# Kernel tuning notes

Hardware: AMD Instinct MI355X
Metric: run time of the kernel (lower is better)

## Reference

```python
import jax, jax.numpy as jnp
import numpy as np

E = 256        # embed_size
H = 512        # nHidden (== coverage d)
EN_V = 32000   # en_vocab
HI_V = 32000   # hi_vocab
S = 96         # source length
T = 96         # target length


def setup_inputs() -> dict:
    key = jax.random.key(0)
    ks = jax.random.split(key, 26)
    def p(k, shape, scale=0.05):
        return jax.random.normal(k, shape, dtype=jnp.float32) * scale
    return dict(
        in_seq=jax.random.randint(ks[0], (S,), 0, EN_V),
        out_seq=jax.random.randint(ks[1], (T,), 0, HI_V),
        enc_embed=p(ks[2], (EN_V, E)),
        dec_embed=p(ks[3], (HI_V, E)),
        # encoder bidirectional GRU (forward / backward directions)
        Wih_f=p(ks[4], (3 * H, E)), Whh_f=p(ks[5], (3 * H, H)), bih_f=p(ks[6], (3 * H,)), bhh_f=p(ks[7], (3 * H,)),
        Wih_b=p(ks[8], (3 * H, E)), Whh_b=p(ks[9], (3 * H, H)), bih_b=p(ks[10], (3 * H,)), bhh_b=p(ks[11], (3 * H,)),
        # decoder GRU (input E + 2H)
        Wih_d=p(ks[12], (3 * H, E + 2 * H)), Whh_d=p(ks[13], (3 * H, H)), bih_d=p(ks[14], (3 * H,)), bhh_d=p(ks[15], (3 * H,)),
        # coverage tanh-RNN (input 3H -> H)
        Wih_c=p(ks[16], (H, 3 * H)), Whh_c=p(ks[17], (H, H)), bih_c=p(ks[18], (H,)), bhh_c=p(ks[19], (H,)),
        # attention params
        va=p(ks[20], (H,)), wa=p(ks[21], (H, H)), ua=p(ks[22], (H, 2 * H)), vc=p(ks[23], (H, H)),
        # output projection (2H + H -> hi_vocab)
        lin_W=p(ks[24], (HI_V, 3 * H)), lin_b=p(ks[25], (HI_V,)),
    )


def _gru_cell(x, h, Wih, Whh, bih, bhh):
    # torch GRU gate order: r, z, n
    gi = Wih @ x + bih
    gh = Whh @ h + bhh
    ir, iz, in_ = jnp.split(gi, 3)
    hr, hz, hn = jnp.split(gh, 3)
    r = jax.nn.sigmoid(ir + hr)
    z = jax.nn.sigmoid(iz + hz)
    n = jnp.tanh(in_ + r * hn)
    return (1.0 - z) * n + z * h


def _forward(in_seq, out_seq, enc_embed, dec_embed,
             Wih_f, Whh_f, bih_f, bhh_f, Wih_b, Whh_b, bih_b, bhh_b,
             Wih_d, Whh_d, bih_d, bhh_d, Wih_c, Whh_c, bih_c, bhh_c,
             va, wa, ua, vc, lin_W, lin_b):
    x_enc = enc_embed[in_seq]                      # (S, E)
    h0 = jnp.zeros((H,), x_enc.dtype)

    def f_step(h, x):
        h2 = _gru_cell(x, h, Wih_f, Whh_f, bih_f, bhh_f)
        return h2, h2

    def b_step(h, x):
        h2 = _gru_cell(x, h, Wih_b, Whh_b, bih_b, bhh_b)
        return h2, h2

    h_fwd, out_f = jax.lax.scan(f_step, h0, x_enc)
    _, out_b = jax.lax.scan(b_step, h0, x_enc[::-1])
    enc = jnp.concatenate([out_f, out_b[::-1]], axis=-1)   # (S, 2H)
    ua_enc = enc @ ua.T                                     # (S, H), reused every step

    def attention(dec_h, cov_vec):
        pre = wa @ dec_h + ua_enc                           # (S, H)
        if cov_vec is not None:
            pre = pre + cov_vec @ vc.T
        e = jnp.tanh(pre) @ va                              # (S,)
        alpha = jax.nn.softmax(e)
        ctx = alpha @ enc                                   # (2H,)
        return ctx, alpha

    def coverage(dec_h, alpha, cov_last):
        # per-position input: alpha_s * [enc_s ; dec_h]  -> (S, 3H)
        inp = alpha[:, None] * jnp.concatenate(
            [enc, jnp.broadcast_to(dec_h, (S, H))], axis=-1)

        def c_step(h, x):
            h2 = jnp.tanh(Wih_c @ x + bih_c + Whh_c @ h + bhh_c)
            return h2, h2

        h_last, outs = jax.lax.scan(c_step, jnp.zeros((H,), inp.dtype), inp)
        # drop last output, prepend previous last_coverage, tanh (as in source)
        cov_vec = jnp.tanh(jnp.concatenate([cov_last[None, :], outs[:-1]], axis=0))
        return cov_vec, h_last

    dec_emb = dec_embed[out_seq]                            # (T, E)

    # --- initial decode step (uses encoder final forward hidden) ---
    h_enc = h_fwd
    ctx0, alpha0 = attention(h_enc, None)
    x0 = jnp.concatenate([ctx0, dec_emb[0]])
    h1 = _gru_cell(x0, h_enc, Wih_d, Whh_d, bih_d, bhh_d)
    out0 = lin_W @ jnp.concatenate([h1, ctx0]) + lin_b
    # note: source discards h1 for the loop; coverage also uses the encoder hidden
    cov_vec0, cov_last0 = coverage(h_enc, alpha0, jnp.zeros((H,), enc.dtype))

    def dec_step(carry, emb):
        h, cov_last, cov_vec = carry
        ctx, alpha = attention(h, cov_vec)
        x = jnp.concatenate([ctx, emb])
        h2 = _gru_cell(x, h, Wih_d, Whh_d, bih_d, bhh_d)
        logits = lin_W @ jnp.concatenate([h2, ctx]) + lin_b
        cov_vec2, cov_last2 = coverage(h2, alpha, cov_last)
        return (h2, cov_last2, cov_vec2), logits

    _, outs = jax.lax.scan(dec_step, (h_enc, cov_last0, cov_vec0), dec_emb[1:])
    return jnp.concatenate([out0[None, :], outs], axis=0)   # (T, HI_V)


def reference(in_seq, out_seq, enc_embed, dec_embed,
              Wih_f, Whh_f, bih_f, bhh_f, Wih_b, Whh_b, bih_b, bhh_b,
              Wih_d, Whh_d, bih_d, bhh_d, Wih_c, Whh_c, bih_c, bhh_c,
              va, wa, ua, vc, lin_W, lin_b):
    return _forward(in_seq, out_seq, enc_embed, dec_embed,
                    Wih_f, Whh_f, bih_f, bhh_f, Wih_b, Whh_b, bih_b, bhh_b,
                    Wih_d, Whh_d, bih_d, bhh_d, Wih_c, Whh_c, bih_c, bhh_c,
                    va, wa, ua, vc, lin_W, lin_b)
```

## Files before the change

kernel.cpp:

```cpp
#include <hip/hip_runtime.h>
#include <hip/hip_bf16.h>
#include <hip/hip_fp16.h>
#include <math.h>

#define CS 96
#define CT 96
#define CE 256
#define CH 512
#define CH2 1024
#define CH3 1536
#define CV 32000
#define CXD 1280

typedef unsigned int u32;
typedef unsigned short u16;
typedef unsigned long long u64;
typedef __attribute__((ext_vector_type(4))) int i32x4;

__device__ __forceinline__ float sigm(float x){ return 1.f/(1.f+expf(-x)); }

__device__ __forceinline__ float dot2f(u32 a, u32 b, float c){
#if __has_builtin(__builtin_amdgcn_fdot2)
  typedef _Float16 hv2 __attribute__((ext_vector_type(2)));
  hv2 x = __builtin_bit_cast(hv2, a), y = __builtin_bit_cast(hv2, b);
  return __builtin_amdgcn_fdot2(x, y, c, false);
#else
  __half2 x = __builtin_bit_cast(__half2, a), y = __builtin_bit_cast(__half2, b);
  return c + __half2float(x.x)*__half2float(y.x) + __half2float(x.y)*__half2float(y.y);
#endif
}

__device__ __forceinline__ u32 packh2(float a, float b){
  return (u32)__half_as_ushort(__float2half(a)) | ((u32)__half_as_ushort(__float2half(b)) << 16);
}

__device__ __forceinline__ float spinf(const u64* p, u32 want){
  u64 x; int g = 0;
  do { x = __hip_atomic_load(p, __ATOMIC_RELAXED, __HIP_MEMORY_SCOPE_AGENT); }
  while ((u32)(x>>32) < want && ++g < 200000);
  return __uint_as_float((u32)x);
}
__device__ __forceinline__ void tagstore(u64* p, u32 tag, float v){
  __hip_atomic_store(p, ((u64)tag<<32) | (u64)__float_as_uint(v),
                     __ATOMIC_RELAXED, __HIP_MEMORY_SCOPE_AGENT);
}

#define COVBAR() do{ asm volatile("s_waitcnt lgkmcnt(0)" ::: "memory"); \
                     __builtin_amdgcn_sched_barrier(0); \
                     __builtin_amdgcn_s_barrier(); \
                     __builtin_amdgcn_sched_barrier(0); }while(0)

__global__ void k_init(u64* tags, int ntags, float* cov_last){
  int i = blockIdx.x*blockDim.x + threadIdx.x;
  int stride = gridDim.x*blockDim.x;
  for (int j=i; j<ntags; j+=stride) tags[j] = 0ull;
  for (int j=i; j<CH; j+=stride) cov_last[j] = 0.f;
}

__global__ void k_embed(const int* iseq, const int* oseq, const float* ee, const float* de,
                        float* x_enc, float* x_dec){
  int s = blockIdx.x, d = threadIdx.x;
  x_enc[s*CE+d] = ee[(long)iseq[s]*CE + d];
  x_dec[s*CE+d] = de[(long)oseq[s]*CE + d];
}

__global__ void k_gi(const float* Wf, const float* bf, const float* Wb, const float* bb,
                     const float* x_enc, float* gf, float* gb){
  int idx = blockIdx.x*256 + threadIdx.x;
  int dir = idx / (CS*CH3);
  int rem = idx - dir*(CS*CH3);
  int s = rem / CH3, r = rem - s*CH3;
  const float* W = dir ? Wb : Wf;
  const float* b = dir ? bb : bf;
  const float* x = x_enc + s*CE;
  const float* w = W + (long)r*CE;
  float acc = b[r];
  #pragma unroll 8
  for (int k=0;k<CE;k++) acc += w[k]*x[k];
  (dir ? gb : gf)[s*CH3 + r] = acc;
}

__launch_bounds__(512)
__global__ void k_enc_f(const float* Whf, const float* bhf, const float* Whb, const float* bhb,
                        const float* gf, const float* gb, float* outf, float* outb, u64* hx){
  int b = blockIdx.x, tid = threadIdx.x;
  int dir = b >> 3;
  const float* Whh = dir ? Whb : Whf;
  const float* bhh = dir ? bhb : bhf;
  const float* gi  = dir ? gb : gf;
  float* o = dir ? outb : outf;
  u64* hxd = hx + (size_t)dir*CH;
  int jl = (b&7)*64 + (tid>>3);
  int part = tid&7, c0 = part*64;
  __shared__ float hl[CH];

  for (int s=0;s<CS;s++){
    if (s > 0){
      if (tid < 64){
        #pragma unroll
        for (int i=0;i<8;i++){ int idx = i*64+tid; hl[idx] = spinf(&hxd[idx], (u32)s); }
      }
      __syncthreads();
    }
    int pos = dir ? (CS-1-s) : s;
    float ar=0.f, az=0.f, an=0.f;
    if (s > 0){
      const float* wr = Whh + (size_t)jl*CH;
      const float* wz = Whh + (size_t)(jl+CH)*CH;
      const float* wn = Whh + (size_t)(jl+2*CH)*CH;
      #pragma unroll 4
      for (int k=c0;k<c0+64;k++){
        float h = hl[k];
        ar += wr[k]*h; az += wz[k]*h; an += wn[k]*h;
      }
    }
    ar += __shfl_xor(ar,1); ar += __shfl_xor(ar,2); ar += __shfl_xor(ar,4);
    az += __shfl_xor(az,1); az += __shfl_xor(az,2); az += __shfl_xor(az,4);
    an += __shfl_xor(an,1); an += __shfl_xor(an,2); an += __shfl_xor(an,4);
    if (part == 0){
      const float* g = gi + pos*CH3;
      float hpj = (s>0) ? hl[jl] : 0.f;
      float r = sigm(g[jl]       + ar + bhh[jl]);
      float z = sigm(g[jl+CH]    + az + bhh[jl+CH]);
      float n = tanhf(g[jl+2*CH] + r*(an + bhh[jl+2*CH]));
      float h = (1.f-z)*n + z*hpj;
      o[pos*CH + jl] = h;
      tagstore(&hxd[jl], (u32)(s+1), h);
    }
    __syncthreads();
  }
}

__global__ void k_prep2(const float* ua, const float* Wic, const float* outf, const float* outb,
                        float* ua_enc, float* Aenc, float* h_carry){
  int idx = blockIdx.x*256 + threadIdx.x;
  if (idx < 2*CS*CH){
    int which = idx / (CS*CH);
    int rem = idx - which*(CS*CH);
    int s = rem / CH, r = rem - s*CH;
    const float* of = outf + s*CH;
    const float* ob = outb + s*CH;
    const float* w = which ? (Wic + (long)r*CH3) : (ua + (long)r*CH2);
    float acc = 0.f;
    #pragma unroll 4
    for (int k=0;k<CH;k++) acc += w[k]*of[k];
    #pragma unroll 4
    for (int k=0;k<CH;k++) acc += w[CH+k]*ob[k];
    (which ? Aenc : ua_enc)[s*CH + r] = acc;
  } else if (idx < 2*CS*CH + CH){
    int j = idx - 2*CS*CH;
    h_carry[j] = outf[(CS-1)*CH + j];
  }
}

__global__ void k_cvt(const float* w, u16* o, int n){
  int i = blockIdx.x*blockDim.x + threadIdx.x;
  int stride = gridDim.x*blockDim.x;
  for (; i<n; i+=stride){
    union { float f; u32 u; } v; v.f = w[i];
    u32 r = (v.u + 0x7fffu + ((v.u>>16)&1u)) >> 16;
    o[i] = (u16)r;
  }
}

__global__ void k_cvt_cov(const float* Wic, u32* wic16P){
  int i = blockIdx.x*256 + threadIdx.x;
  int kp = i >> 9, r = i & 511;
  float a = Wic[(size_t)r*CH3 + CH2 + 2*kp];
  float b = Wic[(size_t)r*CH3 + CH2 + 2*kp + 1];
  wic16P[(size_t)kp*512 + r] = packh2(a, b);
}

__global__ void k_quant(const float* Whc, uint4* w8m, float* rs){
  int r = blockIdx.x;
  int l = threadIdx.x;
  const float* wr = Whc + (size_t)r*CH;
  float m = 0.f;
  for (int k=l; k<CH; k+=64) m = fmaxf(m, fabsf(wr[k]));
  for (int d=1; d<64; d<<=1) m = fmaxf(m, __shfl_xor(m,d));
  float sc = (m > 0.f) ? (127.f/m) : 0.f;
  if (l < 32){
    int kb = l>>2, q = l&3;
    u32 wv[4];
    #pragma unroll
    for (int wi=0;wi<4;wi++){
      u32 p = 0;
      #pragma unroll
      for (int j=0;j<4;j++){
        int v = (int)rintf(wr[kb*64 + q*16 + wi*4 + j]*sc);
        v = max(-127, min(127, v));
        p |= (u32)(v & 255) << (8*j);
      }
      wv[wi] = p;
    }
    int tile = (r>>4)*8 + kb;
    int lane = q*16 + (r&15);
    w8m[(size_t)tile*64 + lane] = make_uint4(wv[0],wv[1],wv[2],wv[3]);
  }
  if (l==0) rs[r] = m/(127.f*127.f);
}

__global__ void k_wah(const float* wa, const float* h, float* wah){
  int j = blockIdx.x*64 + (threadIdx.x>>2);
  int c0 = (threadIdx.x&3)*128;
  const float* w = wa + (long)j*CH;
  float acc = 0.f;
  #pragma unroll 4
  for (int k=c0;k<c0+128;k++) acc += w[k]*h[k];
  acc += __shfl_xor(acc,1); acc += __shfl_xor(acc,2);
  if ((threadIdx.x&3)==0) wah[j] = acc;
}

__global__ void k_attn0(const float* va, const float* ua_enc, const float* wah, float* e){
  int s = blockIdx.x, tid = threadIdx.x;
  __shared__ float red[4];
  float sum = 0.f;
  #pragma unroll
  for (int jj=0;jj<2;jj++){
    int j = tid + jj*256;
    float acc = ua_enc[s*CH + j] + wah[j];
    sum += va[j]*tanhf(acc);
  }
  for (int m=1;m<64;m<<=1) sum += __shfl_xor(sum,m);
  if ((tid&63)==0) red[tid>>6] = sum;
  __syncthreads();
  if (tid==0) e[s] = red[0]+red[1]+red[2]+red[3];
}

template<int BF16>
__launch_bounds__(512, 2)
__global__ void k_step(int t, const void* Wv, const float* lb, const float* hE,
                       u64* hc64, const float* x_dec,
                       const float* eR, float* eW,
                       const float* outf, const float* outb,
                       const float* wa, const float* vc, const float* va, const float* ua_enc,
                       const float* Wid, const float* bid, const float* Whd, const float* bhd,
                       const uint4* w8m, const float* rs, const u32* wic16P,
                       const float* bic, const float* bhc, const float* Aenc,
                       u64* cv64, float* cov_last, float* out){
  int b = blockIdx.x, tid = threadIdx.x;
  u32 wantH = (u32)(t+1);
  u64* hcW = hc64 + (size_t)(t&1)*CH;
  const u64* hcR = hc64 + (size_t)((t+1)&1)*CH;

  __shared__ float el[CS], al[CS];
  __shared__ float ctxl[CH2];
  __shared__ float hl[CH];
  __shared__ float he2[CH];
  __shared__ float red[8];
  __shared__ u32 part_l[CH];
  __shared__ __align__(16) u32 h8w[128];
  __shared__ u32 hd16[256];
  __shared__ float cvsl[CH];

  if (tid < CS) el[tid] = eR[tid];
  __syncthreads();
  if (tid == 0){
    float m = -1e30f;
    for (int s=0;s<CS;s++) m = fmaxf(m, el[s]);
    float sm = 0.f;
    for (int s=0;s<CS;s++){ float ex = expf(el[s]-m); al[s] = ex; sm += ex; }
    float inv = 1.f/sm;
    for (int s=0;s<CS;s++) al[s] *= inv;
  }
  __syncthreads();
  if (b != 0){
    float a0=0.f, a1=0.f;
    for (int s=0;s<CS;s++){ a0 += al[s]*outf[s*CH+tid]; a1 += al[s]*outb[s*CH+tid]; }
    ctxl[tid] = a0; ctxl[CH+tid] = a1;
  }

  if (b == 0){
    if (t == 0){ if (tid < CH) hl[tid] = hE[tid]; }
    else if (tid < 64){
      #pragma unroll
      for (int i=0;i<8;i++){ int idx=i*64+tid; hl[idx] = spinf(&hcW[idx], wantH); }
    }
    __syncthreads();
    if (tid < 256) hd16[tid] = packh2(hl[2*tid], hl[2*tid+1]);
    __syncthreads();
    float bacc_r = 0.f;
    {
      const u32* bw = wic16P + tid;
      #pragma unroll 8
      for (int kp=0;kp<256;kp++)
        bacc_r = dot2f(bw[(size_t)kp*512], hd16[kp], bacc_r);
    }
    i32x4 af[4][8];
    {
      int w = tid>>6, l = tid&63;
      const i32x4* wp = (const i32x4*)w8m;
      #pragma unroll
      for (int j=0;j<4;j++){
        #pragma unroll
        for (int kb=0;kb<8;kb++)
          af[j][kb] = wp[((size_t)((4*w+j)*8+kb))*64 + l];
        asm volatile("" ::: "memory");
      }
    }
    float bsum_r = bic[tid] + bhc[tid];
    float rs_r = rs[tid];
    float a_next = Aenc[tid];
    tagstore(&cv64[tid], wantH, tanhf(cov_last[tid]));
    __syncthreads();

    int w = tid>>6, l = tid&63;
    for (int s=0;s<CS;s++){
      if (s > 0){
        i32x4 acc0={0,0,0,0}, acc1={0,0,0,0}, acc2={0,0,0,0}, acc3={0,0,0,0};
        #pragma unroll
        for (int kb=0;kb<8;kb++){
          i32x4 bfr = *(const i32x4*)&h8w[kb*16 + (l>>4)*4];
          acc0 = __builtin_amdgcn_mfma_i32_16x16x64_i8(af[0][kb], bfr, acc0, 0,0,0);
          acc1 = __builtin_amdgcn_mfma_i32_16x16x64_i8(af[1][kb], bfr, acc1, 0,0,0);
          acc2 = __builtin_amdgcn_mfma_i32_16x16x64_i8(af[2][kb], bfr, acc2, 0,0,0);
          acc3 = __builtin_amdgcn_mfma_i32_16x16x64_i8(af[3][kb], bfr, acc3, 0,0,0);
        }
        if ((l & 15) == 0){
          int rq = l >> 4;
          *(i32x4*)&part_l[(4*w+0)*16 + rq*4] = acc0;
          *(i32x4*)&part_l[(4*w+1)*16 + rq*4] = acc1;
          *(i32x4*)&part_l[(4*w+2)*16 + rq*4] = acc2;
          *(i32x4*)&part_l[(4*w+3)*16 + rq*4] = acc3;
        }
      }
      COVBAR();
      {
        float T = (s > 0) ? (float)(int)part_l[tid] * rs_r : 0.f;
        float a_cur = a_next;
        if (s < CS-1) a_next = Aenc[(s+1)*CH + tid];
        float h = tanhf(T + al[s]*(a_cur + bacc_r) + bsum_r);
        if (s < CS-1){
          int q = (int)rintf(h * 127.f);
          u32 bq = (u32)(q & 255);
          u32 p01 = bq | (__shfl_xor(bq,1) << 8);
          u32 p = p01 | (__shfl_xor(p01,2) << 16);
          if ((tid & 3) == 0) h8w[tid >> 2] = p;
          tagstore(&cv64[(size_t)(s+1)*CH + tid], wantH, tanhf(h));
        } else {
          cov_last[tid] = h;
        }
      }
      COVBAR();
    }
    return;
  }

  if (b >= 97){
    if (t <= 1){ if (tid < CH) he2[tid] = hE[tid]; }
    else       { if (tid < CH) he2[tid] = __uint_as_float((u32)hcR[tid]); }
    __syncthreads();
    {
      int j = (b-97)*16 + (tid>>5);
      int ln = tid&31;
      const float* xd = x_dec + t*CE;
      float ar=0.f, az=0.f, an=0.f;
      {
        int c0 = ln*40;
        const float* wr = Wid + (size_t)j*CXD;
        const float* wz = Wid + (size_t)(j+CH)*CXD;
        const float* wn = Wid + (size_t)(j+2*CH)*CXD;
        for (int k=c0;k<c0+40;k++){
          float x = (k<CH2) ? ctxl[k] : xd[k-CH2];
          ar += wr[k]*x; az += wz[k]*x; an += wn[k]*x;
        }
      }
      float hr=0.f, hz=0.f, hn2=0.f;
      {
        int c0 = ln*16;
        const float* wr = Whd + (size_t)j*CH;
        const float* wz = Whd + (size_t)(j+CH)*CH;
        const float* wn = Whd + (size_t)(j+2*CH)*CH;
        for (int k=c0;k<c0+16;k++){
          float hv = he2[k];
          hr += wr[k]*hv; hz += wz[k]*hv; hn2 += wn[k]*hv;
        }
      }
      for (int m=1;m<32;m<<=1){
        ar+=__shfl_xor(ar,m); az+=__shfl_xor(az,m); an+=__shfl_xor(an,m);
        hr+=__shfl_xor(hr,m); hz+=__shfl_xor(hz,m); hn2+=__shfl_xor(hn2,m);
      }
      if (ln==0){
        float hprev = he2[j];
        float r = sigm(ar + bid[j]       + hr + bhd[j]);
        float z = sigm(az + bid[j+CH]    + hz + bhd[j+CH]);
        float n = tanhf(an + bid[j+2*CH] + r*(hn2 + bhd[j+2*CH]));
        tagstore(&hcW[j], wantH, (1.f-z)*n + z*hprev);
      }
    }
    if (tid < 64){
      #pragma unroll
      for (int i=0;i<8;i++){ int idx=i*64+tid; hl[idx] = spinf(&hcW[idx], wantH); }
    }
    __syncthreads();
    {
      int ln = tid&63;
      int gw = (b-97)*8 + (tid>>6);
      float x[24];
      #pragma unroll
      for (int k=0;k<24;k++){
        int c = k*64 + ln;
        x[k] = (c<CH) ? hl[c] : ctxl[c];
      }
      #pragma unroll
      for (int k=0;k<24;k++){
        int c = k*64 + ln;
        x[k] = (c<CH) ? hl[c] : ctxl[c-CH];
      }
      for (int r=24000+gw; r<CV; r+=256){
        float acc = 0.f;
        if (BF16){
          const u16* w = (const u16*)Wv + (size_t)r*CH3;
          #pragma unroll
          for (int k=0;k<24;k++){
            u32 u = (u32)w[k*64+ln] << 16;
            acc += __uint_as_float(u)*x[k];
          }
        } else {
          const float* w = (const float*)Wv + (size_t)r*CH3;
          #pragma unroll
          for (int k=0;k<24;k++) acc += w[k*64+ln]*x[k];
        }
        for (int m=1;m<64;m<<=1) acc += __shfl_xor(acc,m);
        if (ln==0) out[(size_t)t*CV + r] = acc + lb[r];
      }
    }
    return;
  }

  int s = b - 1;
  if (t == 0){ if (tid < CH) he2[tid] = hE[tid]; }
  if (tid < 64){
    #pragma unroll
    for (int i=0;i<8;i++){ int idx=i*64+tid; hl[idx] = spinf(&hcW[idx], wantH); }
  }
  __syncthreads();
  {
    int ln = tid&63;
    int gw = (b-1)*8 + (tid>>6);
    float x[24];
    #pragma unroll
    for (int k=0;k<24;k++){
      int c = k*64 + ln;
      x[k] = (c<CH) ? hl[c] : ctxl[c-CH];
    }
    for (int r=gw; r<24000; r+=768){
      float acc = 0.f;
      if (BF16){
        const u16* w = (const u16*)Wv + (size_t)r*CH3;
        #pragma unroll
        for (int k=0;k<24;k++){
          u32 u = (u32)w[k*64+ln] << 16;
          acc += __uint_as_float(u)*x[k];
        }
      } else {
        const float* w = (const float*)Wv + (size_t)r*CH3;
        #pragma unroll
        for (int k=0;k<24;k++) acc += w[k*64+ln]*x[k];
      }
      for (int m=1;m<64;m<<=1) acc += __shfl_xor(acc,m);
      if (ln==0) out[(size_t)t*CV + r] = acc + lb[r];
    }
  }
  if (tid < 64){
    #pragma unroll
    for (int i=0;i<8;i++){ int idx=i*64+tid; cvsl[idx] = spinf(&cv64[(size_t)s*CH+idx], wantH); }
  }
  __syncthreads();
  {
    int j = tid;
    const float* hw = (t==0) ? he2 : hl;
    const float* wr = wa + (size_t)j*CH;
    float wacc = 0.f;
    #pragma unroll 4
    for (int k=0;k<CH;k++) wacc += wr[k]*hw[k];
    float acc = ua_enc[s*CH + j] + wacc;
    const float* v = vc + (size_t)j*CH;
    #pragma unroll 4
    for (int k=0;k<CH;k++) acc += v[k]*cvsl[k];
    float val = va[j]*tanhf(acc);
    for (int m=1;m<64;m<<=1) val += __shfl_xor(val,m);
    if ((tid&63)==0) red[tid>>6] = val;
    __syncthreads();
    if (tid==0){
      float sm = 0.f;
      #pragma unroll
      for (int i=0;i<8;i++) sm += red[i];
      eW[s] = sm;
    }
  }
}

extern "C" void kernel_launch(void* const* d_in, const int* in_sizes, int n_in,
                              void* d_out, int out_size, void* d_ws, size_t ws_size,
                              hipStream_t stream){
  (void)in_sizes; (void)n_in; (void)out_size;
  const int*   iseq = (const int*)d_in[0];
  const int*   oseq = (const int*)d_in[1];
  const float* ee   = (const float*)d_in[2];
  const float* de   = (const float*)d_in[3];
  const float* Wih_f=(const float*)d_in[4];  const float* Whh_f=(const float*)d_in[5];
  const float* bih_f=(const float*)d_in[6];  const float* bhh_f=(const float*)d_in[7];
  const float* Wih_b=(const float*)d_in[8];  const float* Whh_b=(const float*)d_in[9];
  const float* bih_b=(const float*)d_in[10]; const float* bhh_b=(const float*)d_in[11];
  const float* Wih_d=(const float*)d_in[12]; const float* Whh_d=(const float*)d_in[13];
  const float* bih_d=(const float*)d_in[14]; const float* bhh_d=(const float*)d_in[15];
  const float* Wih_c=(const float*)d_in[16]; const float* Whh_c=(const float*)d_in[17];
  const float* bih_c=(const float*)d_in[18]; const float* bhh_c=(const float*)d_in[19];
  const float* va   =(const float*)d_in[20]; const float* wa   =(const float*)d_in[21];
  const float* ua   =(const float*)d_in[22]; const float* vc   =(const float*)d_in[23];
  const float* lin_W=(const float*)d_in[24]; const float* lin_b=(const float*)d_in[25];
  float* out = (float*)d_out;
  char* ws = (char*)d_ws;

  size_t off = 0;
  auto A = [&](size_t bytes){ size_t r = off; off = (off + bytes + 255) & ~(size_t)255; return r; };
  size_t o_w8m   = A((size_t)CH*128*4);
  size_t o_rs    = A((size_t)CH*4);
  size_t o_wicP  = A((size_t)256*512*4);
  size_t o_tags  = A((size_t)(1024 + 1024 + CS*CH)*8);
  size_t o_xenc = A((size_t)CS*CE*4), o_xdec = A((size_t)CT*CE*4);
  size_t o_gf   = A((size_t)CS*CH3*4), o_gb  = A((size_t)CS*CH3*4);
  size_t o_of   = A((size_t)CS*CH*4),  o_ob  = A((size_t)CS*CH*4);
  size_t o_uae  = A((size_t)CS*CH*4),  o_Ae  = A((size_t)CS*CH*4);
  size_t o_e0   = A(CS*4), o_e1 = A(CS*4);
  size_t o_hE   = A(CH*4), o_cl = A(CH*4);
  size_t o_wah  = A(CH*4);
  size_t o_lwb  = A((size_t)CV*CH3*2);
  bool use16 = (off <= ws_size);

  uint4* w8m = (uint4*)(ws+o_w8m);    float* rs = (float*)(ws+o_rs);
  u32* wic16P = (u32*)(ws+o_wicP);
  u64* tags = (u64*)(ws+o_tags);
  u64* hx   = tags;
  u64* hc64 = tags + 1024;
  u64* cv64 = tags + 2048;
  int ntags = 1024 + 1024 + CS*CH;
  float* x_enc = (float*)(ws+o_xenc); float* x_dec = (float*)(ws+o_xdec);
  float* gf = (float*)(ws+o_gf);      float* gb = (float*)(ws+o_gb);
  float* outf = (float*)(ws+o_of);    float* outb = (float*)(ws+o_ob);
  float* ua_enc = (float*)(ws+o_uae); float* Aenc = (float*)(ws+o_Ae);
  float* eb0 = (float*)(ws+o_e0);     float* eb1 = (float*)(ws+o_e1);
  float* hE = (float*)(ws+o_hE);      float* cov_last = (float*)(ws+o_cl);
  float* wah = (float*)(ws+o_wah);
  u16* lwb = (u16*)(ws+o_lwb);

  k_init<<<64,256,0,stream>>>(tags, ntags, cov_last);
  k_embed<<<CS,256,0,stream>>>(iseq, oseq, ee, de, x_enc, x_dec);
  k_gi<<<(2*CS*CH3)/256,256,0,stream>>>(Wih_f,bih_f,Wih_b,bih_b,x_enc,gf,gb);
  k_cvt_cov<<<(256*512)/256,256,0,stream>>>(Wih_c, wic16P);
  k_quant<<<CH,64,0,stream>>>(Whh_c, w8m, rs);
  if (use16)
    k_cvt<<<2048,256,0,stream>>>(lin_W, lwb, CV*CH3);
  k_enc_f<<<16,512,0,stream>>>(Whh_f,bhh_f,Whh_b,bhh_b, gf,gb, outf,outb, hx);
  k_prep2<<<(2*CS*CH+CH)/256,256,0,stream>>>(ua, Wih_c, outf, outb, ua_enc, Aenc, hE);
  k_wah<<<8,256,0,stream>>>(wa, hE, wah);
  k_attn0<<<CS,256,0,stream>>>(va, ua_enc, wah, eb0);

  const void* Wv = use16 ? (const void*)lwb : (const void*)lin_W;
  for (int t=0;t<CT;t++){
    const float* eR = (t&1) ? eb1 : eb0;
    float*       eW = (t&1) ? eb0 : eb1;
    if (use16)
      k_step<1><<<129,512,0,stream>>>(t, Wv, lin_b, hE, hc64, x_dec, eR, eW,
                                      outf, outb, wa, vc, va, ua_enc,
                                      Wih_d, bih_d, Whh_d, bhh_d,
                                      w8m, rs, wic16P, bih_c, bhh_c, Aenc,
                                      cv64, cov_last, out);
    else
      k_step<0><<<129,512,0,stream>>>(t, Wv, lin_b, hE, hc64, x_dec, eR, eW,
                                      outf, outb, wa, vc, va, ua_enc,
                                      Wih_d, bih_d, Whh_d, bhh_d,
                                      w8m, rs, wic16P, bih_c, bhh_c, Aenc,
                                      cv64, cov_last, out);
  }
}
```

Before: 23.88 ms.

## Fuse per-timestep decoder launches into one persistent kernel with tagged flags

Replaces 96 separate k_step launches with a single persistent k_dec kernel of 256 blocks that loops over timesteps. Cross-step dependencies go through tagged atomic flags (attention energies now stored as tagged u64 values, hidden state read by spinning). The int8 coverage weight fragments are loaded into registers once instead of every step, and the output-projection rows are split across more blocks. The encoder recurrence also switches to float4 loads with a padded shared hidden buffer. This removes per-step launch and kernel-boundary overhead, but relies on all 256 blocks being co-resident and on spin-wait correctness; the spin limit is also halved.

```diff
diff --git a/kernel.cpp b/kernel.cpp
--- a/kernel.cpp
+++ b/kernel.cpp
@@ -37,7 +37,7 @@
 __device__ __forceinline__ float spinf(const u64* p, u32 want){
   u64 x; int g = 0;
   do { x = __hip_atomic_load(p, __ATOMIC_RELAXED, __HIP_MEMORY_SCOPE_AGENT); }
-  while ((u32)(x>>32) < want && ++g < 200000);
+  while ((u32)(x>>32) < want && ++g < 100000);
   return __uint_as_float((u32)x);
 }
 __device__ __forceinline__ void tagstore(u64* p, u32 tag, float v){
@@ -92,26 +92,30 @@
   u64* hxd = hx + (size_t)dir*CH;
   int jl = (b&7)*64 + (tid>>3);
   int part = tid&7, c0 = part*64;
-  __shared__ float hl[CH];
+  __shared__ __align__(16) float hl[544];
 
   for (int s=0;s<CS;s++){
     if (s > 0){
       if (tid < 64){
         #pragma unroll
-        for (int i=0;i<8;i++){ int idx = i*64+tid; hl[idx] = spinf(&hxd[idx], (u32)s); }
+        for (int i=0;i<8;i++) hl[i*68+tid] = spinf(&hxd[i*64+tid], (u32)s);
       }
       __syncthreads();
     }
     int pos = dir ? (CS-1-s) : s;
     float ar=0.f, az=0.f, an=0.f;
     if (s > 0){
-      const float* wr = Whh + (size_t)jl*CH;
-      const float* wz = Whh + (size_t)(jl+CH)*CH;
-      const float* wn = Whh + (size_t)(jl+2*CH)*CH;
-      #pragma unroll 4
-      for (int k=c0;k<c0+64;k++){
-        float h = hl[k];
-        ar += wr[k]*h; az += wz[k]*h; an += wn[k]*h;
+      const float4* wr = (const float4*)(Whh + (size_t)jl*CH + c0);
+      const float4* wz = (const float4*)(Whh + (size_t)(jl+CH)*CH + c0);
+      const float4* wn = (const float4*)(Whh + (size_t)(jl+2*CH)*CH + c0);
+      const float4* hp = (const float4*)&hl[part*68];
+      #pragma unroll
+      for (int k=0;k<16;k++){
+        float4 h = hp[k];
+        float4 a = wr[k], z = wz[k], n = wn[k];
+        ar += a.x*h.x + a.y*h.y + a.z*h.z + a.w*h.w;
+        az += z.x*h.x + z.y*h.y + z.z*h.z + z.w*h.w;
+        an += n.x*h.x + n.y*h.y + n.z*h.z + n.w*h.w;
       }
     }
     ar += __shfl_xor(ar,1); ar += __shfl_xor(ar,2); ar += __shfl_xor(ar,4);
@@ -119,7 +123,7 @@
     an += __shfl_xor(an,1); an += __shfl_xor(an,2); an += __shfl_xor(an,4);
     if (part == 0){
       const float* g = gi + pos*CH3;
-      float hpj = (s>0) ? hl[jl] : 0.f;
+      float hpj = (s>0) ? hl[jl + ((jl>>6)<<2)] : 0.f;
       float r = sigm(g[jl]       + ar + bhh[jl]);
       float z = sigm(g[jl+CH]    + az + bhh[jl+CH]);
       float n = tanhf(g[jl+2*CH] + r*(an + bhh[jl+2*CH]));
@@ -211,7 +215,7 @@
   if ((threadIdx.x&3)==0) wah[j] = acc;
 }
 
-__global__ void k_attn0(const float* va, const float* ua_enc, const float* wah, float* e){
+__global__ void k_attn0(const float* va, const float* ua_enc, const float* wah, u64* e64){
   int s = blockIdx.x, tid = threadIdx.x;
   __shared__ float red[4];
   float sum = 0.f;
@@ -224,24 +228,20 @@
   for (int m=1;m<64;m<<=1) sum += __shfl_xor(sum,m);
   if ((tid&63)==0) red[tid>>6] = sum;
   __syncthreads();
-  if (tid==0) e[s] = red[0]+red[1]+red[2]+red[3];
+  if (tid==0) tagstore(&e64[s], 1u, red[0]+red[1]+red[2]+red[3]);
 }
 
 template<int BF16>
 __launch_bounds__(512, 2)
-__global__ void k_step(int t, const void* Wv, const float* lb, const float* hE,
-                       u64* hc64, const float* x_dec,
-                       const float* eR, float* eW,
-                       const float* outf, const float* outb,
-                       const float* wa, const float* vc, const float* va, const float* ua_enc,
-                       const float* Wid, const float* bid, const float* Whd, const float* bhd,
-                       const uint4* w8m, const float* rs, const u32* wic16P,
-                       const float* bic, const float* bhc, const float* Aenc,
-                       u64* cv64, float* cov_last, float* out){
+__global__ void k_dec(const void* Wv, const float* lb, const float* hE,
+                      u64* hc64, const float* x_dec, u64* e64,
+                      const float* outf, const float* outb,
+                      const float* wa, const float* vc, const float* va, const float* ua_enc,
+                      const float* Wid, const float* bid, const float* Whd, const float* bhd,
+                      const uint4* w8m, const float* rs, const u32* wic16P,
+                      const float* bic, const float* bhc, const float* Aenc,
+                      u64* cv64, float* cov_last, float* out){
   int b = blockIdx.x, tid = threadIdx.x;
-  u32 wantH = (u32)(t+1);
-  u64* hcW = hc64 + (size_t)(t&1)*CH;
-  const u64* hcR = hc64 + (size_t)((t+1)&1)*CH;
 
   __shared__ float el[CS], al[CS];
   __shared__ float ctxl[CH2];
@@ -253,240 +253,297 @@
   __shared__ u32 hd16[256];
   __shared__ float cvsl[CH];
 
-  if (tid < CS) el[tid] = eR[tid];
-  __syncthreads();
-  if (tid == 0){
-    float m = -1e30f;
-    for (int s=0;s<CS;s++) m = fmaxf(m, el[s]);
-    float sm = 0.f;
-    for (int s=0;s<CS;s++){ float ex = expf(el[s]-m); al[s] = ex; sm += ex; }
-    float inv = 1.f/sm;
-    for (int s=0;s<CS;s++) al[s] *= inv;
+  if (tid < CH) he2[tid] = hE[tid];
+
+  i32x4 af[4][8];
+  if (b == 0){
+    int w = tid>>6, l = tid&63;
+    const i32x4* wp = (const i32x4*)w8m;
+    #pragma unroll
+    for (int j=0;j<4;j++){
+      #pragma unroll
+      for (int kb=0;kb<8;kb++)
+        af[j][kb] = wp[((size_t)((4*w+j)*8+kb))*64 + l];
+      asm volatile("" ::: "memory");
+    }
   }
   __syncthreads();
-  if (b != 0){
-    float a0=0.f, a1=0.f;
-    for (int s=0;s<CS;s++){ a0 += al[s]*outf[s*CH+tid]; a1 += al[s]*outb[s*CH+tid]; }
-    ctxl[tid] = a0; ctxl[CH+tid] = a1;
-  }
-
-  if (b == 0){
-    if (t == 0){ if (tid < CH) hl[tid] = hE[tid]; }
-    else if (tid < 64){
-      #pragma unroll
-      for (int i=0;i<8;i++){ int idx=i*64+tid; hl[idx] = spinf(&hcW[idx], wantH); }
-    }
+
+  for (int t=0;t<CT;t++){
+    u32 wantH = (u32)(t+1);
+    u64* hcW = hc64 + (size_t)(t&1)*CH;
+    const u64* hcR = hc64 + (size_t)((t+1)&1)*CH;
+    const u64* eR = e64 + (size_t)(t&1)*CS;
+    u64* eW = e64 + (size_t)((t+1)&1)*CS;
+
+    if (tid < CS) el[tid] = spinf(&eR[tid], wantH);
     __syncthreads();
-    if (tid < 256) hd16[tid] = packh2(hl[2*tid], hl[2*tid+1]);
+    if (tid == 0){
+      float m = -1e30f;
+      for (int s=0;s<CS;s++) m = fmaxf(m, el[s]);
+      float sm = 0.f;
+      for (int s=0;s<CS;s++){ float ex = expf(el[s]-m); al[s] = ex; sm += ex; }
+      float inv = 1.f/sm;
+      for (int s=0;s<CS;s++) al[s] *= inv;
+    }
     __syncthreads();
-    float bacc_r = 0.f;
+
+    if (b == 0){
+      if (t == CT-1) break;
+      if (t == 0){ if (tid < CH) hl[tid] = he2[tid]; }
+      else if (tid < 64){
+        #pragma unroll
+        for (int i=0;i<8;i++){ int idx=i*64+tid; hl[idx] = spinf(&hcW[idx], wantH); }
+      }
+      __syncthreads();
+      if (tid < 256) hd16[tid] = packh2(hl[2*tid], hl[2*tid+1]);
+      __syncthreads();
+      float bacc_r = 0.f;
+      {
+        const u32* bw = wic16P + tid;
+        #pragma unroll 8
+        for (int kp=0;kp<256;kp++)
+          bacc_r = dot2f(bw[(size_t)kp*512], hd16[kp], bacc_r);
+      }
+      float bsum_r = bic[tid] + bhc[tid];
+      float rs_r = rs[tid];
+      float a_next = Aenc[tid];
+      tagstore(&cv64[tid], wantH, tanhf(cov_last[tid]));
+      __syncthreads();
+
+      int w = tid>>6, l = tid&63;
+      for (int s=0;s<CS;s++){
+        if (s > 0){
+          i32x4 acc0={0,0,0,0}, acc1={0,0,0,0}, acc2={0,0,0,0}, acc3={0,0,0,0};
+          #pragma unroll
+          for (int kb=0;kb<8;kb++){
+            i32x4 bfr = *(const i32x4*)&h8w[kb*16 + (l>>4)*4];
+            acc0 = __builtin_amdgcn_mfma_i32_16x16x64_i8(af[0][kb], bfr, acc0, 0,0,0);
+            acc1 = __builtin_amdgcn_mfma_i32_16x16x64_i8(af[1][kb], bfr, acc1, 0,0,0);
+            acc2 = __builtin_amdgcn_mfma_i32_16x16x64_i8(af[2][kb], bfr, acc2, 0,0,0);
+            acc3 = __builtin_amdgcn_mfma_i32_16x16x64_i8(af[3][kb], bfr, acc3, 0,0,0);
+          }
+          if ((l & 15) == 0){
+            int rq = l >> 4;
+            *(i32x4*)&part_l[(4*w+0)*16 + rq*4] = acc0;
+            *(i32x4*)&part_l[(4*w+1)*16 + rq*4] = acc1;
+            *(i32x4*)&part_l[(4*w+2)*16 + rq*4] = acc2;
+            *(i32x4*)&part_l[(4*w+3)*16 + rq*4] = acc3;
+          }
+        }
+        COVBAR();
+        {
+          float T = (s > 0) ? (float)(int)part_l[tid] * rs_r : 0.f;
+          float a_cur = a_next;
+          if (s < CS-1) a_next = Aenc[(s+1)*CH + tid];
+          float h = tanhf(T + al[s]*(a_cur + bacc_r) + bsum_r);
+          if (s < CS-1){
+            int q = (int)rintf(h * 127.f);
+            u32 bq = (u32)(q & 255);
+            u32 p01 = bq | (__shfl_xor(bq,1) << 8);
+            u32 p = p01 | (__shfl_xor(p01,2) << 16);
+            if ((tid & 3) == 0) h8w[tid >> 2] = p;
+            tagstore(&cv64[(size_t)(s+1)*CH + tid], wantH, tanhf(h));
+          } else {
+            cov_last[tid] = h;
+          }
+        }
+        COVBAR();
+      }
+      __syncthreads();
+      continue;
+    }
+
     {
-      const u32* bw = wic16P + tid;
-      #pragma unroll 8
-      for (int kp=0;kp<256;kp++)
-        bacc_r = dot2f(bw[(size_t)kp*512], hd16[kp], bacc_r);
-    }
-    i32x4 af[4][8];
+      float a0=0.f, a1=0.f;
+      for (int s=0;s<CS;s++){ a0 += al[s]*outf[s*CH+tid]; a1 += al[s]*outb[s*CH+tid]; }
+      ctxl[tid] = a0; ctxl[CH+tid] = a1;
+    }
+    __syncthreads();
+
+    if (b >= 97 && b <= 128){
+      if (t >= 2){
+        if (tid < 64){
+          #pragma unroll
+          for (int i=0;i<8;i++){ int idx=i*64+tid; he2[idx] = spinf(&hcR[idx], (u32)t); }
+        }
+        __syncthreads();
+      }
+      {
+        int j = (b-97)*16 + (tid>>5);
+        int ln = tid&31;
+        const float* xd = x_dec + t*CE;
+        float ar=0.f, az=0.f, an=0.f;
+        {
+          int c0 = ln*40;
+          const float* wr = Wid + (size_t)j*CXD;
+          const float* wz = Wid + (size_t)(j+CH)*CXD;
+          const float* wn = Wid + (size_t)(j+2*CH)*CXD;
+          for (int k=c0;k<c0+40;k++){
+            float x = (k<CH2) ? ctxl[k] : xd[k-CH2];
+            ar += wr[k]*x; az += wz[k]*x; an += wn[k]*x;
+          }
+        }
+        float hr=0.f, hz=0.f, hn2=0.f;
+        {
+          int c0 = ln*16;
+          const float* wr = Whd + (size_t)j*CH;
+          const float* wz = Whd + (size_t)(j+CH)*CH;
+          const float* wn = Whd + (size_t)(j+2*CH)*CH;
+          for (int k=c0;k<c0+16;k++){
+            float hv = he2[k];
+            hr += wr[k]*hv; hz += wz[k]*hv; hn2 += wn[k]*hv;
+          }
+        }
+        for (int m=1;m<32;m<<=1){
+          ar+=__shfl_xor(ar,m); az+=__shfl_xor(az,m); an+=__shfl_xor(an,m);
+          hr+=__shfl_xor(hr,m); hz+=__shfl_xor(hz,m); hn2+=__shfl_xor(hn2,m);
+        }
+        if (ln==0){
+          float hprev = he2[j];
+          float r = sigm(ar + bid[j]       + hr + bhd[j]);
+          float z = sigm(az + bid[j+CH]    + hz + bhd[j+CH]);
+          float n = tanhf(an + bid[j+2*CH] + r*(hn2 + bhd[j+2*CH]));
+          tagstore(&hcW[j], wantH, (1.f-z)*n + z*hprev);
+        }
+      }
+      if (tid < 64){
+        #pragma unroll
+        for (int i=0;i<8;i++){ int idx=i*64+tid; hl[idx] = spinf(&hcW[idx], wantH); }
+      }
+      __syncthreads();
+      {
+        int ln = tid&63;
+        int gw = (b-97)*8 + (tid>>6);
+        float x[24];
+        #pragma unroll
+        for (int k=0;k<24;k++){
+          int c = k*64 + ln;
+          x[k] = (c<CH) ? hl[c] : ctxl[c-CH];
+        }
+        for (int r=12288+gw; r<16384; r+=256){
+          float acc = 0.f;
+          if (BF16){
+            const u16* w = (const u16*)Wv + (size_t)r*CH3;
+            #pragma unroll
+            for (int k=0;k<24;k++){
+              u32 u = (u32)w[k*64+ln] << 16;
+              acc += __uint_as_float(u)*x[k];
+            }
+          } else {
+            const float* w = (const float*)Wv + (size_t)r*CH3;
+            #pragma unroll
+            for (int k=0;k<24;k++) acc += w[k*64+ln]*x[k];
+          }
+          for (int m=1;m<64;m<<=1) acc += __shfl_xor(acc,m);
+          if (ln==0) out[(size_t)t*CV + r] = acc + lb[r];
+        }
+      }
+      __syncthreads();
+      continue;
+    }
+
+    if (b >= 129){
+      if (tid < 64){
+        #pragma unroll
+        for (int i=0;i<8;i++){ int idx=i*64+tid; hl[idx] = spinf(&hcW[idx], wantH); }
+      }
+      __syncthreads();
+      {
+        int ln = tid&63;
+        int gw = (b-129)*8 + (tid>>6);
+        float x[24];
+        #pragma unroll
+        for (int k=0;k<24;k++){
+          int c = k*64 + ln;
+          x[k] = (c<CH) ? hl[c] : ctxl[c-CH];
+        }
+        for (int r=16384+gw; r<CV; r+=1016){
+          float acc = 0.f;
+          if (BF16){
+            const u16* w = (const u16*)Wv + (size_t)r*CH3;
+            #pragma unroll
+            for (int k=0;k<24;k++){
+              u32 u = (u32)w[k*64+ln] << 16;
+              acc += __uint_as_float(u)*x[k];
+            }
+          } else {
+            const float* w = (const float*)Wv + (size_t)r*CH3;
+            #pragma unroll
+            for (int k=0;k<24;k++) acc += w[k*64+ln]*x[k];
+          }
+          for (int m=1;m<64;m<<=1) acc += __shfl_xor(acc,m);
+          if (ln==0) out[(size_t)t*CV + r] = acc + lb[r];
+        }
+      }
+      __syncthreads();
+      continue;
+    }
+
     {
-      int w = tid>>6, l = tid&63;
-      const i32x4* wp = (const i32x4*)w8m;
-      #pragma unroll
-      for (int j=0;j<4;j++){
-        #pragma unroll
-        for (int kb=0;kb<8;kb++)
-          af[j][kb] = wp[((size_t)((4*w+j)*8+kb))*64 + l];
-        asm volatile("" ::: "memory");
-      }
-    }
-    float bsum_r = bic[tid] + bhc[tid];
-    float rs_r = rs[tid];
-    float a_next = Aenc[tid];
-    tagstore(&cv64[tid], wantH, tanhf(cov_last[tid]));
-    __syncthreads();
-
-    int w = tid>>6, l = tid&63;
-    for (int s=0;s<CS;s++){
-      if (s > 0){
-        i32x4 acc0={0,0,0,0}, acc1={0,0,0,0}, acc2={0,0,0,0}, acc3={0,0,0,0};
-        #pragma unroll
-        for (int kb=0;kb<8;kb++){
-          i32x4 bfr = *(const i32x4*)&h8w[kb*16 + (l>>4)*4];
-          acc0 = __builtin_amdgcn_mfma_i32_16x16x64_i8(af[0][kb], bfr, acc0, 0,0,0);
-          acc1 = __builtin_amdgcn_mfma_i32_16x16x64_i8(af[1][kb], bfr, acc1, 0,0,0);
-          acc2 = __builtin_amdgcn_mfma_i32_16x16x64_i8(af[2][kb], bfr, acc2, 0,0,0);
-          acc3 = __builtin_amdgcn_mfma_i32_16x16x64_i8(af[3][kb], bfr, acc3, 0,0,0);
-        }
-        if ((l & 15) == 0){
-          int rq = l >> 4;
-          *(i32x4*)&part_l[(4*w+0)*16 + rq*4] = acc0;
-          *(i32x4*)&part_l[(4*w+1)*16 + rq*4] = acc1;
-          *(i32x4*)&part_l[(4*w+2)*16 + rq*4] = acc2;
-          *(i32x4*)&part_l[(4*w+3)*16 + rq*4] = acc3;
-        }
-      }
-      COVBAR();
+      int s = b - 1;
+      if (tid < 64){
+        #pragma unroll
+        for (int i=0;i<8;i++){ int idx=i*64+tid; hl[idx] = spinf(&hcW[idx], wantH); }
+      }
+      __syncthreads();
       {
-        float T = (s > 0) ? (float)(int)part_l[tid] * rs_r : 0.f;
-        float a_cur = a_next;
-        if (s < CS-1) a_next = Aenc[(s+1)*CH + tid];
-        float h = tanhf(T + al[s]*(a_cur + bacc_r) + bsum_r);
-        if (s < CS-1){
-          int q = (int)rintf(h * 127.f);
-          u32 bq = (u32)(q & 255);
-          u32 p01 = bq | (__shfl_xor(bq,1) << 8);
-          u32 p = p01 | (__shfl_xor(p01,2) << 16);
-          if ((tid & 3) == 0) h8w[tid >> 2] = p;
-          tagstore(&cv64[(size_t)(s+1)*CH + tid], wantH, tanhf(h));
-        } else {
-          cov_last[tid] = h;
-        }
-      }
-      COVBAR();
-    }
-    return;
-  }
-
-  if (b >= 97){
-    if (t <= 1){ if (tid < CH) he2[tid] = hE[tid]; }
-    else       { if (tid < CH) he2[tid] = __uint_as_float((u32)hcR[tid]); }
-    __syncthreads();
-    {
-      int j = (b-97)*16 + (tid>>5);
-      int ln = tid&31;
-      const float* xd = x_dec + t*CE;
-      float ar=0.f, az=0.f, an=0.f;
-      {
-        int c0 = ln*40;
-        const float* wr = Wid + (size_t)j*CXD;
-        const float* wz = Wid + (size_t)(j+CH)*CXD;
-        const float* wn = Wid + (size_t)(j+2*CH)*CXD;
-        for (int k=c0;k<c0+40;k++){
-          float x = (k<CH2) ? ctxl[k] : xd[k-CH2];
-          ar += wr[k]*x; az += wz[k]*x; an += wn[k]*x;
-        }
-      }
-      float hr=0.f, hz=0.f, hn2=0.f;
-      {
-        int c0 = ln*16;
-        const float* wr = Whd + (size_t)j*CH;
-        const float* wz = Whd + (size_t)(j+CH)*CH;
-        const float* wn = Whd + (size_t)(j+2*CH)*CH;
-        for (int k=c0;k<c0+16;k++){
-          float hv = he2[k];
-          hr += wr[k]*hv; hz += wz[k]*hv; hn2 += wn[k]*hv;
-        }
-      }
-      for (int m=1;m<32;m<<=1){
-        ar+=__shfl_xor(ar,m); az+=__shfl_xor(az,m); an+=__shfl_xor(an,m);
-        hr+=__shfl_xor(hr,m); hz+=__shfl_xor(hz,m); hn2+=__shfl_xor(hn2,m);
-      }
-      if (ln==0){
-        float hprev = he2[j];
-        float r = sigm(ar + bid[j]       + hr + bhd[j]);
-        float z = sigm(az + bid[j+CH]    + hz + bhd[j+CH]);
-        float n = tanhf(an + bid[j+2*CH] + r*(hn2 + bhd[j+2*CH]));
-        tagstore(&hcW[j], wantH, (1.f-z)*n + z*hprev);
-      }
-    }
-    if (tid < 64){
-      #pragma unroll
-      for (int i=0;i<8;i++){ int idx=i*64+tid; hl[idx] = spinf(&hcW[idx], wantH); }
-    }
-    __syncthreads();
-    {
-      int ln = tid&63;
-      int gw = (b-97)*8 + (tid>>6);
-      float x[24];
-      #pragma unroll
-      for (int k=0;k<24;k++){
-        int c = k*64 + ln;
-        x[k] = (c<CH) ? hl[c] : ctxl[c];
-      }
-      #pragma unroll
-      for (int k=0;k<24;k++){
-        int c = k*64 + ln;
-        x[k] = (c<CH) ? hl[c] : ctxl[c-CH];
-      }
-      for (int r=24000+gw; r<CV; r+=256){
-        float acc = 0.f;
-        if (BF16){
-          const u16* w = (const u16*)Wv + (size_t)r*CH3;
+        int ln = tid&63;
+        int gw = (b-1)*8 + (tid>>6);
+        float x[24];
+        #pragma unroll
+        for (int k=0;k<24;k++){
+          int c = k*64 + ln;
+          x[k] = (c<CH) ? hl[c] : ctxl[c-CH];
+        }
+        for (int r=gw; r<12288; r+=768){
+          float acc = 0.f;
+          if (BF16){
+            const u16* w = (const u16*)Wv + (size_t)r*CH3;
+            #pragma unroll
+            for (int k=0;k<24;k++){
+              u32 u = (u32)w[k*64+ln] << 16;
+              acc += __uint_as_float(u)*x[k];
+            }
+          } else {
+            const float* w = (const float*)Wv + (size_t)r*CH3;
+            #pragma unroll
+            for (int k=0;k<24;k++) acc += w[k*64+ln]*x[k];
+          }
+          for (int m=1;m<64;m<<=1) acc += __shfl_xor(acc,m);
+          if (ln==0) out[(size_t)t*CV + r] = acc + lb[r];
+        }
+      }
+      if (t < CT-1){
+        if (tid < 64){
           #pragma unroll
-          for (int k=0;k<24;k++){
-            u32 u = (u32)w[k*64+ln] << 16;
-            acc += __uint_as_float(u)*x[k];
-          }
-        } else {
-          const float* w = (const float*)Wv + (size_t)r*CH3;
-          #pragma unroll
-          for (int k=0;k<24;k++) acc += w[k*64+ln]*x[k];
-        }
-        for (int m=1;m<64;m<<=1) acc += __shfl_xor(acc,m);
-        if (ln==0) out[(size_t)t*CV + r] = acc + lb[r];
-      }
-    }
-    return;
-  }
-
-  int s = b - 1;
-  if (t == 0){ if (tid < CH) he2[tid] = hE[tid]; }
-  if (tid < 64){
-    #pragma unroll
-    for (int i=0;i<8;i++){ int idx=i*64+tid; hl[idx] = spinf(&hcW[idx], wantH); }
-  }
-  __syncthreads();
-  {
-    int ln = tid&63;
-    int gw = (b-1)*8 + (tid>>6);
-    float x[24];
-    #pragma unroll
-    for (int k=0;k<24;k++){
-      int c = k*64 + ln;
-      x[k] = (c<CH) ? hl[c] : ctxl[c-CH];
-    }
-    for (int r=gw; r<24000; r+=768){
-      float acc = 0.f;
-      if (BF16){
-        const u16* w = (const u16*)Wv + (size_t)r*CH3;
-        #pragma unroll
-        for (int k=0;k<24;k++){
-          u32 u = (u32)w[k*64+ln] << 16;
-          acc += __uint_as_float(u)*x[k];
-        }
-      } else {
-        const float* w = (const float*)Wv + (size_t)r*CH3;
-        #pragma unroll
-        for (int k=0;k<24;k++) acc += w[k*64+ln]*x[k];
-      }
-      for (int m=1;m<64;m<<=1) acc += __shfl_xor(acc,m);
-      if (ln==0) out[(size_t)t*CV + r] = acc + lb[r];
-    }
-  }
-  if (tid < 64){
-    #pragma unroll
-    for (int i=0;i<8;i++){ int idx=i*64+tid; cvsl[idx] = spinf(&cv64[(size_t)s*CH+idx], wantH); }
-  }
-  __syncthreads();
-  {
-    int j = tid;
-    const float* hw = (t==0) ? he2 : hl;
-    const float* wr = wa + (size_t)j*CH;
-    float wacc = 0.f;
-    #pragma unroll 4
-    for (int k=0;k<CH;k++) wacc += wr[k]*hw[k];
-    float acc = ua_enc[s*CH + j] + wacc;
-    const float* v = vc + (size_t)j*CH;
-    #pragma unroll 4
-    for (int k=0;k<CH;k++) acc += v[k]*cvsl[k];
-    float val = va[j]*tanhf(acc);
-    for (int m=1;m<64;m<<=1) val += __shfl_xor(val,m);
-    if ((tid&63)==0) red[tid>>6] = val;
-    __syncthreads();
-    if (tid==0){
-      float sm = 0.f;
-      #pragma unroll
-      for (int i=0;i<8;i++) sm += red[i];
-      eW[s] = sm;
+          for (int i=0;i<8;i++){ int idx=i*64+tid; cvsl[idx] = spinf(&cv64[(size_t)s*CH+idx], wantH); }
+        }
+        __syncthreads();
+        {
+          int j = tid;
+          const float* hw = (t==0) ? he2 : hl;
+          const float* wr = wa + (size_t)j*CH;
+          float wacc = 0.f;
+          #pragma unroll 4
+          for (int k=0;k<CH;k++) wacc += wr[k]*hw[k];
+          float acc = ua_enc[s*CH + j] + wacc;
+          const float* v = vc + (size_t)j*CH;
+          #pragma unroll 4
+          for (int k=0;k<CH;k++) acc += v[k]*cvsl[k];
+          float val = va[j]*tanhf(acc);
+          for (int m=1;m<64;m<<=1) val += __shfl_xor(val,m);
+          if ((tid&63)==0) red[tid>>6] = val;
+          __syncthreads();
+          if (tid==0){
+            float sm = 0.f;
+            #pragma unroll
+            for (int i=0;i<8;i++) sm += red[i];
+            tagstore(&eW[s], (u32)(t+2), sm);
+          }
+        }
+      }
+      __syncthreads();
     }
   }
 }
@@ -518,12 +575,11 @@
   size_t o_w8m   = A((size_t)CH*128*4);
   size_t o_rs    = A((size_t)CH*4);
   size_t o_wicP  = A((size_t)256*512*4);
-  size_t o_tags  = A((size_t)(1024 + 1024 + CS*CH)*8);
+  size_t o_tags  = A((size_t)(1024 + 1024 + CS*CH + 2*CS)*8);
   size_t o_xenc = A((size_t)CS*CE*4), o_xdec = A((size_t)CT*CE*4);
   size_t o_gf   = A((size_t)CS*CH3*4), o_gb  = A((size_t)CS*CH3*4);
   size_t o_of   = A((size_t)CS*CH*4),  o_ob  = A((size_t)CS*CH*4);
   size_t o_uae  = A((size_t)CS*CH*4),  o_Ae  = A((size_t)CS*CH*4);
-  size_t o_e0   = A(CS*4), o_e1 = A(CS*4);
   size_t o_hE   = A(CH*4), o_cl = A(CH*4);
   size_t o_wah  = A(CH*4);
   size_t o_lwb  = A((size_t)CV*CH3*2);
@@ -535,12 +591,12 @@
   u64* hx   = tags;
   u64* hc64 = tags + 1024;
   u64* cv64 = tags + 2048;
-  int ntags = 1024 + 1024 + CS*CH;
+  u64* e64  = tags + 2048 + CS*CH;
+  int ntags = 1024 + 1024 + CS*CH + 2*CS;
   float* x_enc = (float*)(ws+o_xenc); float* x_dec = (float*)(ws+o_xdec);
   float* gf = (float*)(ws+o_gf);      float* gb = (float*)(ws+o_gb);
   float* outf = (float*)(ws+o_of);    float* outb = (float*)(ws+o_ob);
   float* ua_enc = (float*)(ws+o_uae); float* Aenc = (float*)(ws+o_Ae);
-  float* eb0 = (float*)(ws+o_e0);     float* eb1 = (float*)(ws+o_e1);
   float* hE = (float*)(ws+o_hE);      float* cov_last = (float*)(ws+o_cl);
   float* wah = (float*)(ws+o_wah);
   u16* lwb = (u16*)(ws+o_lwb);
@@ -555,23 +611,17 @@
   k_enc_f<<<16,512,0,stream>>>(Whh_f,bhh_f,Whh_b,bhh_b, gf,gb, outf,outb, hx);
   k_prep2<<<(2*CS*CH+CH)/256,256,0,stream>>>(ua, Wih_c, outf, outb, ua_enc, Aenc, hE);
   k_wah<<<8,256,0,stream>>>(wa, hE, wah);
-  k_attn0<<<CS,256,0,stream>>>(va, ua_enc, wah, eb0);
+  k_attn0<<<CS,256,0,stream>>>(va, ua_enc, wah, e64);
 
   const void* Wv = use16 ? (const void*)lwb : (const void*)lin_W;
-  for (int t=0;t<CT;t++){
-    const float* eR = (t&1) ? eb1 : eb0;
-    float*       eW = (t&1) ? eb0 : eb1;
-    if (use16)
-      k_step<1><<<129,512,0,stream>>>(t, Wv, lin_b, hE, hc64, x_dec, eR, eW,
-                                      outf, outb, wa, vc, va, ua_enc,
-                                      Wih_d, bih_d, Whh_d, bhh_d,
-                                      w8m, rs, wic16P, bih_c, bhh_c, Aenc,
-                                      cv64, cov_last, out);
-    else
-      k_step<0><<<129,512,0,stream>>>(t, Wv, lin_b, hE, hc64, x_dec, eR, eW,
-                                      outf, outb, wa, vc, va, ua_enc,
-                                      Wih_d, bih_d, Whh_d, bhh_d,
-                                      w8m, rs, wic16P, bih_c, bhh_c, Aenc,
-                                      cv64, cov_last, out);
-  }
-}
+  if (use16)
+    k_dec<1><<<256,512,0,stream>>>(Wv, lin_b, hE, hc64, x_dec, e64, outf, outb,
+                                   wa, vc, va, ua_enc, Wih_d, bih_d, Whh_d, bhh_d,
+                                   w8m, rs, wic16P, bih_c, bhh_c, Aenc,
+                                   cv64, cov_last, out);
+  else
+    k_dec<0><<<256,512,0,stream>>>(Wv, lin_b, hE, hc64, x_dec, e64, outf, outb,
+                                   wa, vc, va, ua_enc, Wih_d, bih_d, Whh_d, bhh_d,
+                                   w8m, rs, wic16P, bih_c, bhh_c, Aenc,
+                                   cv64, cov_last, out);
+}
```

Result: slower. 59.41 ms (+148.8%).
